# Optimization experiments

Measured on AMD Instinct MI355X. Metric: run time of the kernel, lower is better.

The kernel has to match this reference:

```python
import jax, jax.numpy as jnp
import numpy as np

D_MODEL, D_FF, D_KEY, D_VALUE, NUM_HEADS = 1024, 4096, 64, 64, 16
EPS = 1e-5
B, S = 2, 2048


def layer_norm(x, gamma, beta):
    # torch x.var() default is unbiased (ddof=1)
    mean = jnp.mean(x, axis=-1, keepdims=True)
    var = jnp.var(x, axis=-1, keepdims=True, ddof=1)
    return (x - mean) / jnp.sqrt(var + EPS) * gamma + beta


def setup_inputs() -> dict:
    key = jax.random.key(0)
    ks = jax.random.split(key, 16)
    s = 0.02
    return {
        "x": jax.random.normal(ks[0], (B, S, D_MODEL), dtype=jnp.float32),
        "mask": jnp.zeros((B, 1, 1, S), dtype=bool),
        "Wq": jax.random.normal(ks[1], (D_MODEL, NUM_HEADS * D_KEY), dtype=jnp.float32) * s,
        "bq": jnp.zeros((NUM_HEADS * D_KEY,), jnp.float32),
        "Wk": jax.random.normal(ks[2], (D_MODEL, NUM_HEADS * D_KEY), dtype=jnp.float32) * s,
        "bk": jnp.zeros((NUM_HEADS * D_KEY,), jnp.float32),
        "Wv": jax.random.normal(ks[3], (D_MODEL, NUM_HEADS * D_VALUE), dtype=jnp.float32) * s,
        "bv": jnp.zeros((NUM_HEADS * D_VALUE,), jnp.float32),
        "Wo": jax.random.normal(ks[4], (NUM_HEADS * D_VALUE, D_MODEL), dtype=jnp.float32) * s,
        "bo": jnp.zeros((D_MODEL,), jnp.float32),
        "gamma1": jnp.ones((D_MODEL,), jnp.float32),
        "beta1": jnp.zeros((D_MODEL,), jnp.float32),
        "W1": jax.random.normal(ks[5], (D_MODEL, D_FF), dtype=jnp.float32) * s,
        "b1": jnp.zeros((D_FF,), jnp.float32),
        "W2": jax.random.normal(ks[6], (D_FF, D_MODEL), dtype=jnp.float32) * s,
        "b2": jnp.zeros((D_MODEL,), jnp.float32),
        "gamma2": jnp.ones((D_MODEL,), jnp.float32),
        "beta2": jnp.zeros((D_MODEL,), jnp.float32),
    }


def reference(x, mask, Wq, bq, Wk, bk, Wv, bv, Wo, bo, gamma1, beta1, W1, b1, W2, b2, gamma2, beta2):
    Bsz, Sq, _ = x.shape
    # ---- multi-head attention (self-attention) ----
    q = (x @ Wq + bq).reshape(Bsz, Sq, NUM_HEADS, D_KEY)
    k = (x @ Wk + bk).reshape(Bsz, Sq, NUM_HEADS, D_KEY)
    v = (x @ Wv + bv).reshape(Bsz, Sq, NUM_HEADS, D_VALUE)
    scores = jnp.einsum("bqhd,bkhd->bhqk", q, k) / jnp.sqrt(jnp.float32(D_KEY))
    scores = jnp.where(mask, -jnp.inf, scores)
    attn = jax.nn.softmax(scores, axis=-1)
    ctx = jnp.einsum("bhqk,bkhd->bqhd", attn, v).reshape(Bsz, Sq, NUM_HEADS * D_VALUE)
    attn_out = ctx @ Wo + bo
    # ---- residual + LN, FFN, residual + LN ----
    h = layer_norm(attn_out + x, gamma1, beta1)
    ff = jnp.maximum(h @ W1 + b1, 0.0) @ W2 + b2
    out = layer_norm(ff + h, gamma2, beta2)
    return out
```

## Files before the change

kernel.cpp:

```cpp
#include <hip/hip_runtime.h>
#include <cstddef>
#include <cstdint>

#define BATCH   2
#define SEQ     2048
#define DMODEL  1024
#define DFF     4096
#define NHEADS  16
#define DHEAD   64
#define NTOK    (BATCH * SEQ)
#define LN_EPS  1e-5f

typedef __attribute__((ext_vector_type(8))) short bf16x8;
typedef __attribute__((ext_vector_type(4))) float f32x4;

#define MFMA(a, b, c) __builtin_amdgcn_mfma_f32_16x16x32_bf16((a), (b), (c), 0, 0, 0)

__device__ __forceinline__ unsigned short f2bf(float f) {
    unsigned int u = __float_as_uint(f);
    u += 0x7fffu + ((u >> 16) & 1u);
    return (unsigned short)(u >> 16);
}

__device__ __forceinline__ void gld_lds16(const void* g, void* l) {
    __builtin_amdgcn_global_load_lds(
        (const __attribute__((address_space(1))) void*)g,
        (__attribute__((address_space(3))) void*)l, 16, 0, 0);
}

template <bool RELU, bool RES, bool OUTBF16>
__global__ __launch_bounds__(256) void gemm_bt(
    const short* __restrict__ A, const short* __restrict__ Bt,
    const float* __restrict__ bias, const float* __restrict__ res,
    void* __restrict__ Cout, int M, int N, int K)
{
    __shared__ __align__(16) short As[128][32];
    __shared__ __align__(16) short Bs[128][32];

    const int tid  = threadIdx.x;
    const int lane = tid & 63;
    const int w    = tid >> 6;
    const int row0 = blockIdx.y * 128;
    const int col0 = blockIdx.x * 128;
    const int wr   = (w >> 1) * 64;
    const int wc   = (w & 1) * 64;
    const int m    = lane & 15;
    const int q    = lane >> 4;

    f32x4 acc[4][4] = {};

    const int sr = w * 32;
    const short* ga = A  + (size_t)(row0 + sr + (lane >> 2)) * K + (lane & 3) * 8;
    const short* gb = Bt + (size_t)(col0 + sr + (lane >> 2)) * K + (lane & 3) * 8;
    short* lA0 = &As[sr][0];
    short* lA1 = &As[sr + 16][0];
    short* lB0 = &Bs[sr][0];
    short* lB1 = &Bs[sr + 16][0];

    for (int k0 = 0; k0 < K; k0 += 32) {
        gld_lds16(ga + k0, lA0);
        gld_lds16(ga + (size_t)16 * K + k0, lA1);
        gld_lds16(gb + k0, lB0);
        gld_lds16(gb + (size_t)16 * K + k0, lB1);
        __syncthreads();

        bf16x8 af[4], bfr[4];
#pragma unroll
        for (int i = 0; i < 4; ++i) af[i]  = *(const bf16x8*)&As[wr + i * 16 + m][q * 8];
#pragma unroll
        for (int i = 0; i < 4; ++i) bfr[i] = *(const bf16x8*)&Bs[wc + i * 16 + m][q * 8];
#pragma unroll
        for (int mi = 0; mi < 4; ++mi)
#pragma unroll
            for (int ni = 0; ni < 4; ++ni)
                acc[mi][ni] = MFMA(af[mi], bfr[ni], acc[mi][ni]);
        __syncthreads();
    }

#pragma unroll
    for (int mi = 0; mi < 4; ++mi) {
#pragma unroll
        for (int ni = 0; ni < 4; ++ni) {
            const int col = col0 + wc + ni * 16 + m;
            const float bv = bias[col];
#pragma unroll
            for (int r = 0; r < 4; ++r) {
                const int row = row0 + wr + mi * 16 + q * 4 + r;
                float v = acc[mi][ni][r] + bv;
                if (RES)  v += res[(size_t)row * N + col];
                if (RELU) v = fmaxf(v, 0.0f);
                if (OUTBF16)
                    ((unsigned short*)Cout)[(size_t)row * N + col] = f2bf(v);
                else
                    ((float*)Cout)[(size_t)row * N + col] = v;
            }
        }
    }
}

__global__ __launch_bounds__(256) void gemm_sk(
    const short* __restrict__ A, const short* __restrict__ Bt,
    const float* __restrict__ bias,
    float* __restrict__ P0, float* __restrict__ P1, int M, int N, int K)
{
    __shared__ __align__(16) short As[128][32];
    __shared__ __align__(16) short Bs[128][32];

    const int tid  = threadIdx.x;
    const int lane = tid & 63;
    const int w    = tid >> 6;
    const int row0 = blockIdx.y * 128;
    const int col0 = blockIdx.x * 128;
    const int z    = blockIdx.z;
    const int KH   = K >> 1;
    const int kofs = z * KH;
    const int wr   = (w >> 1) * 64;
    const int wc   = (w & 1) * 64;
    const int m    = lane & 15;
    const int q    = lane >> 4;

    f32x4 acc[4][4] = {};

    const int sr = w * 32;
    const short* ga = A  + (size_t)(row0 + sr + (lane >> 2)) * K + kofs + (lane & 3) * 8;
    const short* gb = Bt + (size_t)(col0 + sr + (lane >> 2)) * K + kofs + (lane & 3) * 8;
    short* lA0 = &As[sr][0];
    short* lA1 = &As[sr + 16][0];
    short* lB0 = &Bs[sr][0];
    short* lB1 = &Bs[sr + 16][0];

    for (int k0 = 0; k0 < KH; k0 += 32) {
        gld_lds16(ga + k0, lA0);
        gld_lds16(ga + (size_t)16 * K + k0, lA1);
        gld_lds16(gb + k0, lB0);
        gld_lds16(gb + (size_t)16 * K + k0, lB1);
        __syncthreads();

        bf16x8 af[4], bfr[4];
#pragma unroll
        for (int i = 0; i < 4; ++i) af[i]  = *(const bf16x8*)&As[wr + i * 16 + m][q * 8];
#pragma unroll
        for (int i = 0; i < 4; ++i) bfr[i] = *(const bf16x8*)&Bs[wc + i * 16 + m][q * 8];
#pragma unroll
        for (int mi = 0; mi < 4; ++mi)
#pragma unroll
            for (int ni = 0; ni < 4; ++ni)
                acc[mi][ni] = MFMA(af[mi], bfr[ni], acc[mi][ni]);
        __syncthreads();
    }

    float* dst = z ? P1 : P0;
    const float bscale = z ? 0.0f : 1.0f;
#pragma unroll
    for (int mi = 0; mi < 4; ++mi) {
#pragma unroll
        for (int ni = 0; ni < 4; ++ni) {
            const int col = col0 + wc + ni * 16 + m;
            const float bv = bias[col] * bscale;
#pragma unroll
            for (int r = 0; r < 4; ++r) {
                const int row = row0 + wr + mi * 16 + q * 4 + r;
                dst[(size_t)row * N + col] = acc[mi][ni][r] + bv;
            }
        }
    }
}

__global__ __launch_bounds__(256) void gemm_qkv(
    const short* __restrict__ A, const short* __restrict__ Bt,
    const float* __restrict__ bias, short* __restrict__ QKb,
    unsigned short* __restrict__ Vt)
{
    const int K = DMODEL;
    __shared__ __align__(16) short As[128][32];
    __shared__ __align__(16) short Bs[128][32];

    const int tid  = threadIdx.x;
    const int lane = tid & 63;
    const int w    = tid >> 6;
    const int row0 = blockIdx.y * 128;
    const int col0 = blockIdx.x * 128;
    const int wr   = (w >> 1) * 64;
    const int wc   = (w & 1) * 64;
    const int m    = lane & 15;
    const int q    = lane >> 4;

    f32x4 acc[4][4] = {};

    const int sr = w * 32;
    const short* ga = A  + (size_t)(row0 + sr + (lane >> 2)) * K + (lane & 3) * 8;
    const short* gb = Bt + (size_t)(col0 + sr + (lane >> 2)) * K + (lane & 3) * 8;
    short* lA0 = &As[sr][0];
    short* lA1 = &As[sr + 16][0];
    short* lB0 = &Bs[sr][0];
    short* lB1 = &Bs[sr + 16][0];

    for (int k0 = 0; k0 < K; k0 += 32) {
        gld_lds16(ga + k0, lA0);
        gld_lds16(ga + (size_t)16 * K + k0, lA1);
        gld_lds16(gb + k0, lB0);
        gld_lds16(gb + (size_t)16 * K + k0, lB1);
        __syncthreads();
        bf16x8 af[4], bfr[4];
#pragma unroll
        for (int i = 0; i < 4; ++i) af[i]  = *(const bf16x8*)&As[wr + i * 16 + m][q * 8];
#pragma unroll
        for (int i = 0; i < 4; ++i) bfr[i] = *(const bf16x8*)&Bs[wc + i * 16 + m][q * 8];
#pragma unroll
        for (int mi = 0; mi < 4; ++mi)
#pragma unroll
            for (int ni = 0; ni < 4; ++ni)
                acc[mi][ni] = MFMA(af[mi], bfr[ni], acc[mi][ni]);
        __syncthreads();
    }

    const int mode = (col0 >= 2048) ? 2 : (col0 < 1024 ? 0 : 1);
    const float scale = (mode == 0) ? 0.1803368801111204f : 1.0f;
#pragma unroll
    for (int mi = 0; mi < 4; ++mi) {
#pragma unroll
        for (int ni = 0; ni < 4; ++ni) {
            const int col = col0 + wc + ni * 16 + m;
            const float bv = bias[col];
#pragma unroll
            for (int r = 0; r < 4; ++r) {
                const int row = row0 + wr + mi * 16 + q * 4 + r;
                const float v = (acc[mi][ni][r] + bv) * scale;
                if (mode < 2) {
                    QKb[(size_t)row * 2048 + col] = (short)f2bf(v);
                } else {
                    const int hd  = col - 2048;
                    const int bb  = row >> 11;
                    const int key = row & (SEQ - 1);
                    Vt[((size_t)(bb * 1024 + hd)) * SEQ + key] = f2bf(v);
                }
            }
        }
    }
}

__global__ __launch_bounds__(256) void attn_mfma(
    const short* __restrict__ Qp,
    const short* __restrict__ Kp,
    const short* __restrict__ Vtg,
    unsigned short* __restrict__ CTX)
{
    __shared__ __align__(16) short Ks[2][64][64];
    __shared__ __align__(16) short Vs[2][64][64];
    __shared__ __align__(16) short Ps[4][32][64];

    const int tid  = threadIdx.x;
    const int lane = tid & 63;
    const int w    = tid >> 6;
    const int b    = blockIdx.z;
    const int h    = blockIdx.y;
    const int q0   = blockIdx.x * 128;
    const int m    = lane & 15;
    const int qd   = lane >> 4;

    bf16x8 qreg[2][2];
#pragma unroll
    for (int g = 0; g < 2; ++g) {
        const short* gq = Qp + (size_t)(b * SEQ + q0 + w * 32 + g * 16 + m) * 2048 + h * 64;
        qreg[g][0] = *(const bf16x8*)(gq + qd * 8);
        qreg[g][1] = *(const bf16x8*)(gq + (qd + 4) * 8);
    }

    bf16x8 bones;
#pragma unroll
    for (int c = 0; c < 8; ++c) bones[c] = (short)0x3F80;

    const int cg = (lane & 7) ^ (lane >> 3);
    const short* Kg = Kp  + (size_t)(b * SEQ) * 2048 + h * 64 + cg * 8;
    const short* Vg = Vtg + (size_t)(b * 1024 + h * 64) * SEQ + cg * 8;

    {
        const short* gk = Kg + (size_t)(w * 16 + (lane >> 3)) * 2048;
        gld_lds16(gk,            &Ks[0][w * 16][0]);
        gld_lds16(gk + 8 * 2048, &Ks[0][w * 16 + 8][0]);
        const short* gv = Vg + (size_t)(w * 16 + (lane >> 3)) * SEQ;
        gld_lds16(gv,            &Vs[0][w * 16][0]);
        gld_lds16(gv + 8 * SEQ,  &Vs[0][w * 16 + 8][0]);
    }

    f32x4 lacc[2] = {};
    f32x4 oacc[2][4] = {};

    for (int j = 0; j < SEQ / 64; ++j) {
        const int cur = j & 1;
        __syncthreads();
        if (j + 1 < SEQ / 64) {
            const int nb = 1 - cur;
            const short* gk = Kg + (size_t)((j + 1) * 64 + w * 16 + (lane >> 3)) * 2048;
            gld_lds16(gk,            &Ks[nb][w * 16][0]);
            gld_lds16(gk + 8 * 2048, &Ks[nb][w * 16 + 8][0]);
            const short* gv = Vg + (size_t)(w * 16 + (lane >> 3)) * SEQ + (j + 1) * 64;
            gld_lds16(gv,            &Vs[nb][w * 16][0]);
            gld_lds16(gv + 8 * SEQ,  &Vs[nb][w * 16 + 8][0]);
        }

        f32x4 sacc[2][4] = {};
#pragma unroll
        for (int ks = 0; ks < 2; ++ks) {
            const int kc = ks * 4 + qd;
#pragma unroll
            for (int ni = 0; ni < 4; ++ni) {
                const int kn = ni * 16 + m;
                bf16x8 bk = *(const bf16x8*)&Ks[cur][kn][(kc ^ (kn & 7)) * 8];
                sacc[0][ni] = MFMA(qreg[0][ks], bk, sacc[0][ni]);
                sacc[1][ni] = MFMA(qreg[1][ks], bk, sacc[1][ni]);
            }
        }

#pragma unroll
        for (int g = 0; g < 2; ++g)
#pragma unroll
            for (int ni = 0; ni < 4; ++ni)
#pragma unroll
                for (int r = 0; r < 4; ++r) {
                    const float p = __builtin_amdgcn_exp2f(sacc[g][ni][r]);
                    const int row = g * 16 + qd * 4 + r;
                    const int swc = (ni * 2 + (m >> 3)) ^ (row & 7);
                    Ps[w][row][swc * 8 + (m & 7)] = (short)(__float_as_uint(p) >> 16);
                }

#pragma unroll
        for (int ks = 0; ks < 2; ++ks) {
            const int kc = ks * 4 + qd;
            bf16x8 ap0 = *(const bf16x8*)&Ps[w][m][(kc ^ (m & 7)) * 8];
            bf16x8 ap1 = *(const bf16x8*)&Ps[w][16 + m][(kc ^ (m & 7)) * 8];
            lacc[0] = MFMA(ap0, bones, lacc[0]);
            lacc[1] = MFMA(ap1, bones, lacc[1]);
#pragma unroll
            for (int ni = 0; ni < 4; ++ni) {
                const int dn = ni * 16 + m;
                bf16x8 bv = *(const bf16x8*)&Vs[cur][dn][(kc ^ (dn & 7)) * 8];
                oacc[0][ni] = MFMA(ap0, bv, oacc[0][ni]);
                oacc[1][ni] = MFMA(ap1, bv, oacc[1][ni]);
            }
        }
    }

#pragma unroll
    for (int g = 0; g < 2; ++g) {
        float inv[4];
#pragma unroll
        for (int r = 0; r < 4; ++r) inv[r] = 1.0f / lacc[g][r];
#pragma unroll
        for (int ni = 0; ni < 4; ++ni)
#pragma unroll
            for (int r = 0; r < 4; ++r) {
                const int row = q0 + w * 32 + g * 16 + qd * 4 + r;
                const int col = h * 64 + ni * 16 + m;
                CTX[(size_t)(b * SEQ + row) * DMODEL + col] = f2bf(oacc[g][ni][r] * inv[r]);
            }
    }
}

__global__ __launch_bounds__(256) void prep(
    const float* __restrict__ x,
    const float* __restrict__ Wq, const float* __restrict__ Wk,
    const float* __restrict__ Wv, const float* __restrict__ Wo,
    const float* __restrict__ W1, const float* __restrict__ W2,
    const float* __restrict__ bq, const float* __restrict__ bk,
    const float* __restrict__ bv,
    short* __restrict__ xb, short* __restrict__ Wqkvt, short* __restrict__ Wot,
    short* __restrict__ W1t, short* __restrict__ W2t, float* __restrict__ bqkv)
{
    __shared__ float t[32][33];
    const int id  = blockIdx.x;
    const int tid = threadIdx.x;

    if (id < 4096) {
        const size_t i = ((size_t)id * 256 + tid) * 4;
        const float4 v = *(const float4*)(x + i);
        short4 o;
        o.x = (short)f2bf(v.x); o.y = (short)f2bf(v.y);
        o.z = (short)f2bf(v.z); o.w = (short)f2bf(v.w);
        *(short4*)(xb + i) = o;
        return;
    }
    if (id >= 16384) {
        const int i = (id - 16384) * 256 + tid;
        bqkv[i] = (i < 1024) ? bq[i] : (i < 2048 ? bk[i - 1024] : bv[i - 2048]);
        return;
    }

    const float* W; short* Wt; int K, N, bx, by;
    if (id < 8192) {
        const int i2 = id - 4096;
        W = W1; Wt = W1t; K = 1024; N = 4096;
        bx = (i2 & 127) * 32; by = (i2 >> 7) * 32;
    } else if (id < 12288) {
        const int i2 = id - 8192;
        W = W2; Wt = W2t; K = 4096; N = 1024;
        bx = (i2 & 31) * 32; by = (i2 >> 5) * 32;
    } else {
        const int i2 = id - 12288;
        const int z = i2 >> 10, i3 = i2 & 1023;
        W  = (z == 0) ? Wq : (z == 1) ? Wk : (z == 2) ? Wv : Wo;
        Wt = (z == 3) ? Wot : (Wqkvt + (size_t)z * 1024 * 1024);
        K = 1024; N = 1024;
        bx = (i3 & 31) * 32; by = (i3 >> 5) * 32;
    }
    const int c = tid & 31, r8 = tid >> 5;
#pragma unroll
    for (int i = 0; i < 4; ++i)
        t[r8 + i * 8][c] = W[(size_t)(by + r8 + i * 8) * N + bx + c];
    __syncthreads();
#pragma unroll
    for (int i = 0; i < 4; ++i)
        Wt[(size_t)(bx + r8 + i * 8) * K + by + c] = (short)f2bf(t[c][r8 + i * 8]);
}

template <bool BF16OUT>
__global__ __launch_bounds__(256) void ln_comb(
    const float* __restrict__ P0, const float* __restrict__ P1,
    const float* __restrict__ res,
    const float* __restrict__ gamma, const float* __restrict__ beta,
    float* __restrict__ Y, short* __restrict__ Yb)
{
    const int row = blockIdx.x;
    const int tid = threadIdx.x;
    __shared__ float red[256];

    const float4 p0 = ((const float4*)(P0  + (size_t)row * DMODEL))[tid];
    const float4 p1 = ((const float4*)(P1  + (size_t)row * DMODEL))[tid];
    const float4 rv = ((const float4*)(res + (size_t)row * DMODEL))[tid];
    float4 xv;
    xv.x = p0.x + p1.x + rv.x;
    xv.y = p0.y + p1.y + rv.y;
    xv.z = p0.z + p1.z + rv.z;
    xv.w = p0.w + p1.w + rv.w;

    red[tid] = xv.x + xv.y + xv.z + xv.w;
    __syncthreads();
    for (int st = 128; st > 0; st >>= 1) {
        if (tid < st) red[tid] += red[tid + st];
        __syncthreads();
    }
    const float mean = red[0] / (float)DMODEL;
    __syncthreads();

    const float dx0 = xv.x - mean, dx1 = xv.y - mean;
    const float dx2 = xv.z - mean, dx3 = xv.w - mean;
    red[tid] = dx0 * dx0 + dx1 * dx1 + dx2 * dx2 + dx3 * dx3;
    __syncthreads();
    for (int st = 128; st > 0; st >>= 1) {
        if (tid < st) red[tid] += red[tid + st];
        __syncthreads();
    }
    const float var = red[0] / (float)(DMODEL - 1);
    const float rs = rsqrtf(var + LN_EPS);

    const float4 gv = ((const float4*)gamma)[tid];
    const float4 bv = ((const float4*)beta)[tid];
    float4 o;
    o.x = dx0 * rs * gv.x + bv.x;
    o.y = dx1 * rs * gv.y + bv.y;
    o.z = dx2 * rs * gv.z + bv.z;
    o.w = dx3 * rs * gv.w + bv.w;
    ((float4*)(Y + (size_t)row * DMODEL))[tid] = o;
    if (BF16OUT) {
        short4 ob;
        ob.x = (short)f2bf(o.x); ob.y = (short)f2bf(o.y);
        ob.z = (short)f2bf(o.z); ob.w = (short)f2bf(o.w);
        *(short4*)(Yb + (size_t)row * DMODEL + tid * 4) = ob;
    }
}

extern "C" void kernel_launch(void* const* d_in, const int* in_sizes, int n_in,
                              void* d_out, int out_size, void* d_ws, size_t ws_size,
                              hipStream_t stream)
{
    const float* x   = (const float*)d_in[0];
    const float* Wq  = (const float*)d_in[2];
    const float* bq  = (const float*)d_in[3];
    const float* Wk  = (const float*)d_in[4];
    const float* bk  = (const float*)d_in[5];
    const float* Wv  = (const float*)d_in[6];
    const float* bv  = (const float*)d_in[7];
    const float* Wo  = (const float*)d_in[8];
    const float* bo  = (const float*)d_in[9];
    const float* g1  = (const float*)d_in[10];
    const float* be1 = (const float*)d_in[11];
    const float* W1  = (const float*)d_in[12];
    const float* b1  = (const float*)d_in[13];
    const float* W2  = (const float*)d_in[14];
    const float* b2  = (const float*)d_in[15];
    const float* g2  = (const float*)d_in[16];
    const float* be2 = (const float*)d_in[17];
    float* out = (float*)d_out;
    char*  ws  = (char*)d_ws;
    (void)in_sizes; (void)n_in; (void)out_size; (void)ws_size;

    const size_t MB = 1ull << 20;
    short* xb    = (short*)(ws);
    short* W1t   = (short*)(ws + 8 * MB);
    short* W2t   = (short*)(ws + 16 * MB);
    short* Wqkvt = (short*)(ws + 24 * MB);
    short* Wot   = (short*)(ws + 30 * MB);
    float* bqkv  = (float*)(ws + 32 * MB);
    short* QKb   = (short*)(ws + 33 * MB);
    unsigned short* Vtg = (unsigned short*)(ws + 49 * MB);
    unsigned short* CTX = (unsigned short*)(ws + 57 * MB);
    float* PA0   = (float*)(ws + 33 * MB);
    float* hF    = (float*)(ws + 33 * MB);
    short* Hb    = (short*)(ws);
    float* PF0   = (float*)(ws);
    short* F1    = (short*)(ws + 49 * MB);

    dim3 blk(256);

    prep<<<dim3(16396), blk, 0, stream>>>(x, Wq, Wk, Wv, Wo, W1, W2, bq, bk, bv,
                                          xb, Wqkvt, Wot, W1t, W2t, bqkv);

    gemm_qkv<<<dim3(3072 / 128, NTOK / 128), blk, 0, stream>>>(xb, Wqkvt, bqkv, QKb, Vtg);

    attn_mfma<<<dim3(SEQ / 128, NHEADS, BATCH), blk, 0, stream>>>(
        QKb, QKb + 1024, (const short*)Vtg, CTX);

    gemm_sk<<<dim3(DMODEL / 128, NTOK / 128, 2), blk, 0, stream>>>(
        (const short*)CTX, Wot, bo, PA0, out, NTOK, DMODEL, DMODEL);
    ln_comb<true><<<NTOK, blk, 0, stream>>>(PA0, out, x, g1, be1, hF, Hb);

    gemm_bt<true, false, true><<<dim3(DFF / 128, NTOK / 128), blk, 0, stream>>>(
        Hb, W1t, b1, nullptr, F1, NTOK, DFF, DMODEL);

    gemm_sk<<<dim3(DMODEL / 128, NTOK / 128, 2), blk, 0, stream>>>(
        F1, W2t, b2, PF0, out, NTOK, DMODEL, DFF);
    ln_comb<false><<<NTOK, blk, 0, stream>>>(PF0, out, hF, g2, be2, out, nullptr);
}
```

Measured before the change: 388.4 us.

## Split attention over key halves and use 128x64 split-K GEMM tiles

Attention now splits the key range into two halves per query tile, which doubles the block count. Each half writes unnormalized fp32 partial outputs and row sums, and a new combine kernel merges them into bf16 context. The split-K GEMMs move to 128x64 tiles with a 64-wide K step and a swizzled LDS layout, again for more blocks and fewer barriers. The cost is an extra kernel launch plus extra fp32 traffic (two 16MB partials) for the attention combine.

```diff
diff --git a/kernel.cpp b/kernel.cpp
--- a/kernel.cpp
+++ b/kernel.cpp
@@ -98,64 +98,70 @@
     }
 }
 
-__global__ __launch_bounds__(256) void gemm_sk(
+__global__ __launch_bounds__(256) void gemm_sk64(
     const short* __restrict__ A, const short* __restrict__ Bt,
     const float* __restrict__ bias,
     float* __restrict__ P0, float* __restrict__ P1, int M, int N, int K)
 {
-    __shared__ __align__(16) short As[128][32];
-    __shared__ __align__(16) short Bs[128][32];
+    __shared__ __align__(16) short As[128][64];
+    __shared__ __align__(16) short Bs[64][64];
 
     const int tid  = threadIdx.x;
     const int lane = tid & 63;
     const int w    = tid >> 6;
     const int row0 = blockIdx.y * 128;
-    const int col0 = blockIdx.x * 128;
+    const int col0 = blockIdx.x * 64;
     const int z    = blockIdx.z;
     const int KH   = K >> 1;
     const int kofs = z * KH;
-    const int wr   = (w >> 1) * 64;
-    const int wc   = (w & 1) * 64;
+    const int wr   = w * 32;
     const int m    = lane & 15;
     const int q    = lane >> 4;
 
-    f32x4 acc[4][4] = {};
-
-    const int sr = w * 32;
-    const short* ga = A  + (size_t)(row0 + sr + (lane >> 2)) * K + kofs + (lane & 3) * 8;
-    const short* gb = Bt + (size_t)(col0 + sr + (lane >> 2)) * K + kofs + (lane & 3) * 8;
-    short* lA0 = &As[sr][0];
-    short* lA1 = &As[sr + 16][0];
-    short* lB0 = &Bs[sr][0];
-    short* lB1 = &Bs[sr + 16][0];
-
-    for (int k0 = 0; k0 < KH; k0 += 32) {
-        gld_lds16(ga + k0, lA0);
-        gld_lds16(ga + (size_t)16 * K + k0, lA1);
-        gld_lds16(gb + k0, lB0);
-        gld_lds16(gb + (size_t)16 * K + k0, lB1);
-        __syncthreads();
-
-        bf16x8 af[4], bfr[4];
-#pragma unroll
-        for (int i = 0; i < 4; ++i) af[i]  = *(const bf16x8*)&As[wr + i * 16 + m][q * 8];
-#pragma unroll
-        for (int i = 0; i < 4; ++i) bfr[i] = *(const bf16x8*)&Bs[wc + i * 16 + m][q * 8];
-#pragma unroll
-        for (int mi = 0; mi < 4; ++mi)
-#pragma unroll
-            for (int ni = 0; ni < 4; ++ni)
-                acc[mi][ni] = MFMA(af[mi], bfr[ni], acc[mi][ni]);
+    f32x4 acc[2][4] = {};
+
+    const int cg = (lane & 7) ^ ((lane >> 3) & 7);
+    const short* ga = A  + (size_t)(row0 + w * 32 + (lane >> 3)) * K + kofs + cg * 8;
+    const short* gb = Bt + (size_t)(col0 + w * 16 + (lane >> 3)) * K + kofs + cg * 8;
+
+    for (int k0 = 0; k0 < KH; k0 += 64) {
+#pragma unroll
+        for (int i = 0; i < 4; ++i)
+            gld_lds16(ga + (size_t)i * 8 * K + k0, &As[w * 32 + i * 8][0]);
+#pragma unroll
+        for (int i = 0; i < 2; ++i)
+            gld_lds16(gb + (size_t)i * 8 * K + k0, &Bs[w * 16 + i * 8][0]);
+        __syncthreads();
+
+#pragma unroll
+        for (int kk = 0; kk < 2; ++kk) {
+            bf16x8 af[2], bfr[4];
+#pragma unroll
+            for (int i = 0; i < 2; ++i) {
+                const int row = wr + i * 16 + m;
+                af[i] = *(const bf16x8*)&As[row][((kk * 4 + q) ^ (row & 7)) * 8];
+            }
+#pragma unroll
+            for (int i = 0; i < 4; ++i) {
+                const int row = i * 16 + m;
+                bfr[i] = *(const bf16x8*)&Bs[row][((kk * 4 + q) ^ (row & 7)) * 8];
+            }
+#pragma unroll
+            for (int mi = 0; mi < 2; ++mi)
+#pragma unroll
+                for (int ni = 0; ni < 4; ++ni)
+                    acc[mi][ni] = MFMA(af[mi], bfr[ni], acc[mi][ni]);
+        }
         __syncthreads();
     }
 
     float* dst = z ? P1 : P0;
     const float bscale = z ? 0.0f : 1.0f;
 #pragma unroll
-    for (int mi = 0; mi < 4; ++mi) {
+    for (int mi = 0; mi < 2; ++mi) {
 #pragma unroll
         for (int ni = 0; ni < 4; ++ni) {
-            const int col = col0 + wc + ni * 16 + m;
+            const int col = col0 + ni * 16 + m;
             const float bv = bias[col] * bscale;
 #pragma unroll
             for (int r = 0; r < 4; ++r) {
@@ -243,7 +249,8 @@
     const short* __restrict__ Qp,
     const short* __restrict__ Kp,
     const short* __restrict__ Vtg,
-    unsigned short* __restrict__ CTX)
+    float* __restrict__ PO0, float* __restrict__ PO1,
+    float* __restrict__ lbuf)
 {
     __shared__ __align__(16) short Ks[2][64][64];
     __shared__ __align__(16) short Vs[2][64][64];
@@ -252,11 +259,13 @@
     const int tid  = threadIdx.x;
     const int lane = tid & 63;
     const int w    = tid >> 6;
+    const int kv   = blockIdx.x & 1;
+    const int q0   = (blockIdx.x >> 1) * 128;
+    const int h    = blockIdx.y;
     const int b    = blockIdx.z;
-    const int h    = blockIdx.y;
-    const int q0   = blockIdx.x * 128;
     const int m    = lane & 15;
     const int qd   = lane >> 4;
+    const int j0   = kv * 16;
 
     bf16x8 qreg[2][2];
 #pragma unroll
@@ -275,10 +284,10 @@
     const short* Vg = Vtg + (size_t)(b * 1024 + h * 64) * SEQ + cg * 8;
 
     {
-        const short* gk = Kg + (size_t)(w * 16 + (lane >> 3)) * 2048;
+        const short* gk = Kg + (size_t)(j0 * 64 + w * 16 + (lane >> 3)) * 2048;
         gld_lds16(gk,            &Ks[0][w * 16][0]);
         gld_lds16(gk + 8 * 2048, &Ks[0][w * 16 + 8][0]);
-        const short* gv = Vg + (size_t)(w * 16 + (lane >> 3)) * SEQ;
+        const short* gv = Vg + (size_t)(w * 16 + (lane >> 3)) * SEQ + j0 * 64;
         gld_lds16(gv,            &Vs[0][w * 16][0]);
         gld_lds16(gv + 8 * SEQ,  &Vs[0][w * 16 + 8][0]);
     }
@@ -286,10 +295,11 @@
     f32x4 lacc[2] = {};
     f32x4 oacc[2][4] = {};
 
-    for (int j = 0; j < SEQ / 64; ++j) {
-        const int cur = j & 1;
-        __syncthreads();
-        if (j + 1 < SEQ / 64) {
+    for (int jj = 0; jj < 16; ++jj) {
+        const int j   = j0 + jj;
+        const int cur = jj & 1;
+        __syncthreads();
+        if (jj + 1 < 16) {
             const int nb = 1 - cur;
             const short* gk = Kg + (size_t)((j + 1) * 64 + w * 16 + (lane >> 3)) * 2048;
             gld_lds16(gk,            &Ks[nb][w * 16][0]);
@@ -341,20 +351,49 @@
         }
     }
 
+    float* dst = kv ? PO1 : PO0;
 #pragma unroll
     for (int g = 0; g < 2; ++g) {
-        float inv[4];
-#pragma unroll
-        for (int r = 0; r < 4; ++r) inv[r] = 1.0f / lacc[g][r];
 #pragma unroll
         for (int ni = 0; ni < 4; ++ni)
 #pragma unroll
             for (int r = 0; r < 4; ++r) {
                 const int row = q0 + w * 32 + g * 16 + qd * 4 + r;
                 const int col = h * 64 + ni * 16 + m;
-                CTX[(size_t)(b * SEQ + row) * DMODEL + col] = f2bf(oacc[g][ni][r] * inv[r]);
-            }
-    }
+                dst[(size_t)(b * SEQ + row) * DMODEL + col] = oacc[g][ni][r];
+            }
+        if (m == 0) {
+#pragma unroll
+            for (int r = 0; r < 4; ++r) {
+                const int row = q0 + w * 32 + g * 16 + qd * 4 + r;
+                lbuf[(((size_t)kv * BATCH + b) * NHEADS + h) * SEQ + row] = lacc[g][r];
+            }
+        }
+    }
+}
+
+__global__ __launch_bounds__(256) void attn_comb(
+    const float* __restrict__ PO0, const float* __restrict__ PO1,
+    const float* __restrict__ lbuf, unsigned short* __restrict__ CTX)
+{
+    const int row = blockIdx.x;
+    const int tid = threadIdx.x;
+    const int b   = row >> 11;
+    const int s   = row & (SEQ - 1);
+    const int h   = tid >> 4;
+
+    const float l0 = lbuf[(((size_t)0 * BATCH + b) * NHEADS + h) * SEQ + s];
+    const float l1 = lbuf[(((size_t)1 * BATCH + b) * NHEADS + h) * SEQ + s];
+    const float inv = 1.0f / (l0 + l1);
+
+    const float4 o0 = ((const float4*)(PO0 + (size_t)row * DMODEL))[tid];
+    const float4 o1 = ((const float4*)(PO1 + (size_t)row * DMODEL))[tid];
+    short4 o;
+    o.x = (short)f2bf((o0.x + o1.x) * inv);
+    o.y = (short)f2bf((o0.y + o1.y) * inv);
+    o.z = (short)f2bf((o0.z + o1.z) * inv);
+    o.w = (short)f2bf((o0.w + o1.w) * inv);
+    *(short4*)((short*)CTX + (size_t)row * DMODEL + tid * 4) = o;
 }
 
 __global__ __launch_bounds__(256) void prep(
@@ -501,9 +540,11 @@
     short* Wqkvt = (short*)(ws + 24 * MB);
     short* Wot   = (short*)(ws + 30 * MB);
     float* bqkv  = (float*)(ws + 32 * MB);
+    float* lbuf  = (float*)(ws + 32 * MB + 64 * 1024);
     short* QKb   = (short*)(ws + 33 * MB);
     unsigned short* Vtg = (unsigned short*)(ws + 49 * MB);
     unsigned short* CTX = (unsigned short*)(ws + 57 * MB);
+    float* PO0   = (float*)(ws + 65 * MB);
     float* PA0   = (float*)(ws + 33 * MB);
     float* hF    = (float*)(ws + 33 * MB);
     short* Hb    = (short*)(ws);
@@ -517,17 +558,18 @@
 
     gemm_qkv<<<dim3(3072 / 128, NTOK / 128), blk, 0, stream>>>(xb, Wqkvt, bqkv, QKb, Vtg);
 
-    attn_mfma<<<dim3(SEQ / 128, NHEADS, BATCH), blk, 0, stream>>>(
-        QKb, QKb + 1024, (const short*)Vtg, CTX);
-
-    gemm_sk<<<dim3(DMODEL / 128, NTOK / 128, 2), blk, 0, stream>>>(
+    attn_mfma<<<dim3((SEQ / 128) * 2, NHEADS, BATCH), blk, 0, stream>>>(
+        QKb, QKb + 1024, (const short*)Vtg, PO0, out, lbuf);
+    attn_comb<<<dim3(NTOK), blk, 0, stream>>>(PO0, out, lbuf, CTX);
+
+    gemm_sk64<<<dim3(DMODEL / 64, NTOK / 128, 2), blk, 0, stream>>>(
         (const short*)CTX, Wot, bo, PA0, out, NTOK, DMODEL, DMODEL);
     ln_comb<true><<<NTOK, blk, 0, stream>>>(PA0, out, x, g1, be1, hF, Hb);
 
     gemm_bt<true, false, true><<<dim3(DFF / 128, NTOK / 128), blk, 0, stream>>>(
         Hb, W1t, b1, nullptr, F1, NTOK, DFF, DMODEL);
 
-    gemm_sk<<<dim3(DMODEL / 128, NTOK / 128, 2), blk, 0, stream>>>(
+    gemm_sk64<<<dim3(DMODEL / 64, NTOK / 128, 2), blk, 0, stream>>>(
         F1, W2t, b2, PF0, out, NTOK, DMODEL, DFF);
     ln_comb<false><<<NTOK, blk, 0, stream>>>(PF0, out, hF, g2, be2, out, nullptr);
 }
```

After: 379.7 us. 1.02x faster.
